# Optimization experiments

Hardware: AMD Instinct MI355X
Metric: run time of the kernel (lower is better)

The kernel has to match this reference:

```python
import jax, jax.numpy as jnp
import numpy as np


def setup_inputs() -> dict:
    key = jax.random.key(0)
    ks = jax.random.split(key, 8)
    n_src, n_dst, n_edges = 100000, 50000, 600000
    d_in, d_out = 128, 128
    n_reuse, n_cache = 5000, 8000
    full_dst_len = n_dst + n_reuse

    feat_src = jax.random.normal(ks[0], (n_src, d_in), jnp.float32)
    src = jax.random.randint(ks[1], (n_edges,), 0, n_src)
    dst = jax.random.randint(ks[2], (n_edges,), 0, n_dst)
    # xavier-ish init for the two bias-free Linear layers (stored as [out, in] like torch)
    W_self = jax.random.normal(ks[3], (d_out, d_in), jnp.float32) / np.sqrt(d_in).astype(np.float32)
    W_neigh = jax.random.normal(ks[4], (d_out, d_in), jnp.float32) / np.sqrt(d_in).astype(np.float32)
    # reuse_indices must be unique positions within [0, full_dst_len)
    reuse_indices = jnp.sort(jax.random.permutation(ks[5], full_dst_len)[:n_reuse])
    reuse_embedding = jax.random.normal(ks[6], (n_reuse, d_out), jnp.float32)
    cache_indices = jax.random.randint(ks[7], (n_cache,), 0, full_dst_len)
    return dict(feat_src=feat_src, W_self=W_self, W_neigh=W_neigh,
                reuse_embedding=reuse_embedding, src=src, dst=dst,
                reuse_indices=reuse_indices, cache_indices=cache_indices,
                n_dst=n_dst)


def reference(feat_src, W_self, W_neigh, reuse_embedding, src, dst,
              reuse_indices, cache_indices, n_dst):
    # --- GraphSAGE 'mean' aggregation on a block graph ---
    feat_dst = feat_src[:n_dst]                         # [n_dst, D_in]
    msgs = feat_src[src]                                # [E, D_in] copy_src gather
    ssum = jax.ops.segment_sum(msgs, dst, num_segments=n_dst)          # [n_dst, D_in]
    deg = jax.ops.segment_sum(jnp.ones_like(msgs[:, 0]), dst, num_segments=n_dst)
    h_neigh = jnp.where(deg[:, None] > 0, ssum / jnp.maximum(deg, 1.0)[:, None], 0.0)
    rst = feat_dst @ W_self.T + h_neigh @ W_neigh.T     # fc_self + fc_neigh

    # --- cache-reuse scatter merge (flag == 0 path) ---
    n_reuse = reuse_indices.shape[0]
    full_dst_len = n_dst + n_reuse
    keep = jnp.ones((full_dst_len,), dtype=bool).at[reuse_indices].set(False)
    unprune_indices = jnp.nonzero(keep, size=n_dst)[0]  # np.delete equivalent
    full = jnp.zeros((full_dst_len, rst.shape[1]), rst.dtype)
    full = full.at[unprune_indices].set(rst).at[reuse_indices].set(reuse_embedding)
    cache_embedding = jax.lax.stop_gradient(full[cache_indices])  # .detach()
    return full, cache_embedding
```

## Files before the change

### kernel.cpp

```cpp
#include <hip/hip_runtime.h>

#define N_SRC   100000
#define N_DST   50000
#define D       128
#define MAXDEG  64

#define RPB     32
#define NB      1563
#define CHUNKS  256
#define TOTAL_BLOCKS 2048
#define COUNT_BLOCKS 256

typedef __attribute__((ext_vector_type(8))) short bf16x8;
typedef __attribute__((ext_vector_type(4))) float f32x4;

__device__ __forceinline__ unsigned short f2bf(float f) {
    unsigned u = __float_as_uint(f);
    u += 0x7FFFu + ((u >> 16) & 1u);
    return (unsigned short)(u >> 16);
}
__device__ __forceinline__ float bf2f(unsigned short u) {
    return __uint_as_float((unsigned)u << 16);
}

__global__ __launch_bounds__(256)
void prep_count_kernel(const int* __restrict__ dst,
                       int* __restrict__ cntmatT,
                       int n_edges, int cb,
                       const int* __restrict__ reuse_idx,
                       int* __restrict__ rowpos, int n_reuse,
                       const float* __restrict__ Wself,
                       const float* __restrict__ Wneigh,
                       unsigned short* __restrict__ wbf,
                       const float* __restrict__ feat,
                       unsigned int* __restrict__ featbf_u32) {
    __shared__ int lc[NB];
    if (blockIdx.x < COUNT_BLOCKS) {
        for (int i = threadIdx.x; i < NB; i += 256) lc[i] = 0;
        __syncthreads();
        int c = blockIdx.x;
        int e0 = c * cb, e1 = min(n_edges, e0 + cb);
        for (int e = e0 + (int)threadIdx.x; e < e1; e += 256)
            atomicAdd(&lc[dst[e] >> 5], 1);
        __syncthreads();
        for (int i = threadIdx.x; i < NB; i += 256)
            cntmatT[i * CHUNKS + c] = lc[i];
    } else {
        int stid = (blockIdx.x - COUNT_BLOCKS) * 256 + threadIdx.x;
        const int sstride = (TOTAL_BLOCKS - COUNT_BLOCKS) * 256;

        if (stid < N_DST) {
            int lo = 0, hi = n_reuse;
            while (lo < hi) {
                int mid = (lo + hi) >> 1;
                if (reuse_idx[mid] - mid > stid) hi = mid; else lo = mid + 1;
            }
            rowpos[stid] = stid + lo;
        }
        if (stid < 128 * 256) {
            int n = stid >> 8;
            int k = stid & 255;
            float v = (k < 128) ? Wself[n * 128 + k] : Wneigh[n * 128 + (k - 128)];
            wbf[stid] = f2bf(v);
        }
        const int n4 = N_SRC * (D / 4);
        for (int i = stid; i < n4; i += sstride) {
            float4 v = *(const float4*)(feat + (size_t)i * 4);
            uint2 o;
            o.x = (unsigned)f2bf(v.x) | ((unsigned)f2bf(v.y) << 16);
            o.y = (unsigned)f2bf(v.z) | ((unsigned)f2bf(v.w) << 16);
            *(uint2*)(featbf_u32 + (size_t)i * 2) = o;
        }
    }
}

__global__ __launch_bounds__(256)
void bucket_scan_kernel(const int* __restrict__ cntmatT,
                        int* __restrict__ offrel,
                        int* __restrict__ bsum) {
    __shared__ int s[CHUNKS];
    int k = blockIdx.x;
    int t = threadIdx.x;
    int x = cntmatT[k * CHUNKS + t];
    s[t] = x;
    __syncthreads();
#pragma unroll
    for (int off = 1; off < CHUNKS; off <<= 1) {
        int v = (t >= off) ? s[t - off] : 0;
        __syncthreads();
        s[t] += v;
        __syncthreads();
    }
    offrel[k * CHUNKS + t] = s[t] - x;
    if (t == CHUNKS - 1) bsum[k] = s[t];
}

__global__ __launch_bounds__(256)
void base_scan_kernel(const int* __restrict__ bsum,
                      int* __restrict__ bucketbase) {
    const int PER = (NB + 255) / 256;
    __shared__ int part[256];
    int t = threadIdx.x;
    int local[PER];
    int run = 0;
#pragma unroll
    for (int i = 0; i < PER; ++i) {
        int idx = t * PER + i;
        int v = (idx < NB) ? bsum[idx] : 0;
        local[i] = run;
        run += v;
    }
    part[t] = run;
    __syncthreads();
#pragma unroll
    for (int off = 1; off < 256; off <<= 1) {
        int v = (t >= off) ? part[t - off] : 0;
        __syncthreads();
        part[t] += v;
        __syncthreads();
    }
    int segbase = part[t] - run;
#pragma unroll
    for (int i = 0; i < PER; ++i) {
        int idx = t * PER + i;
        if (idx < NB) bucketbase[idx] = segbase + local[i];
    }
    if (t == 255) bucketbase[NB] = part[255];
}

__global__ __launch_bounds__(256)
void scatter_kernel(const int* __restrict__ src,
                    const int* __restrict__ dst,
                    const int* __restrict__ offrel,
                    const int* __restrict__ bucketbase,
                    unsigned int* __restrict__ pe,
                    int n_edges, int cb) {
    __shared__ int lc[NB];
    for (int i = threadIdx.x; i < NB; i += 256) lc[i] = 0;
    __syncthreads();
    int c = blockIdx.x;
    int e0 = c * cb, e1 = min(n_edges, e0 + cb);
    for (int e = e0 + (int)threadIdx.x; e < e1; e += 256) {
        int d = dst[e];
        int s = src[e];
        int k = d >> 5;
        int r = atomicAdd(&lc[k], 1);
        int pos = bucketbase[k] + offrel[k * CHUNKS + c] + r;
        pe[pos] = ((unsigned)s << 5) | (unsigned)(d & 31);
    }
}

__global__ __launch_bounds__(256)
void fine_gather_kernel(const unsigned int* __restrict__ pe,
                        const int* __restrict__ bucketbase,
                        const unsigned short* __restrict__ featbf,
                        uint4* __restrict__ hneigh_u4) {
    __shared__ int lell[RPB * MAXDEG];
    __shared__ int rc[RPB];
    int k = blockIdx.x;
    int tid = threadIdx.x;
    if (tid < RPB) rc[tid] = 0;
    __syncthreads();
    int e0 = bucketbase[k], e1 = bucketbase[k + 1];
    for (int e = e0 + tid; e < e1; e += 256) {
        unsigned p = pe[e];
        int rl = (int)(p & 31u);
        int slot = atomicAdd(&rc[rl], 1);
        if (slot < MAXDEG)
            lell[rl * MAXDEG + slot] = (int)(p >> 5);
    }
    __syncthreads();

    union U { uint4 v; unsigned short us[8]; };
#pragma unroll
    for (int pass = 0; pass < 2; ++pass) {
        int rl   = pass * 16 + (tid >> 4);
        int lane = tid & 15;
        int row  = k * RPB + rl;
        if (row < N_DST) {
            int deg = rc[rl];
            int n = min(deg, MAXDEG);
            float inv = 1.0f / fmaxf((float)deg, 1.0f);
            const int* lst = lell + rl * MAXDEG;

            float acc[8];
#pragma unroll
            for (int q = 0; q < 8; ++q) acc[q] = 0.f;

            int j = 0;
            for (; j + 4 <= n; j += 4) {
                int s0 = lst[j + 0];
                int s1 = lst[j + 1];
                int s2 = lst[j + 2];
                int s3 = lst[j + 3];
                U a, b, c, d;
                a.v = *(const uint4*)(featbf + (size_t)s0 * D + lane * 8);
                b.v = *(const uint4*)(featbf + (size_t)s1 * D + lane * 8);
                c.v = *(const uint4*)(featbf + (size_t)s2 * D + lane * 8);
                d.v = *(const uint4*)(featbf + (size_t)s3 * D + lane * 8);
#pragma unroll
                for (int q = 0; q < 8; ++q)
                    acc[q] += (bf2f(a.us[q]) + bf2f(b.us[q])) + (bf2f(c.us[q]) + bf2f(d.us[q]));
            }
            for (; j < n; ++j) {
                int s = lst[j];
                U a;
                a.v = *(const uint4*)(featbf + (size_t)s * D + lane * 8);
#pragma unroll
                for (int q = 0; q < 8; ++q) acc[q] += bf2f(a.us[q]);
            }
            uint4 o;
            o.x = (unsigned)f2bf(acc[0] * inv) | ((unsigned)f2bf(acc[1] * inv) << 16);
            o.y = (unsigned)f2bf(acc[2] * inv) | ((unsigned)f2bf(acc[3] * inv) << 16);
            o.z = (unsigned)f2bf(acc[4] * inv) | ((unsigned)f2bf(acc[5] * inv) << 16);
            o.w = (unsigned)f2bf(acc[6] * inv) | ((unsigned)f2bf(acc[7] * inv) << 16);
            hneigh_u4[(size_t)row * 16 + lane] = o;
        }
    }
}

__global__ __launch_bounds__(256, 2)
void gemm_kernel(const unsigned short* __restrict__ featbf,
                 const unsigned short* __restrict__ hneigh,
                 const unsigned short* __restrict__ wbf,
                 const int* __restrict__ rowpos,
                 float* __restrict__ full) {
    __shared__ unsigned short Wl[128 * 256];

    int tid = threadIdx.x;
    {
        int n = tid >> 1;
        int ckbase = (tid & 1) * 16;
        const uint4* s = (const uint4*)(wbf + n * 256);
        uint4* d = (uint4*)(Wl + n * 256);
#pragma unroll
        for (int i = 0; i < 16; ++i) {
            int ck = ckbase + i;
            d[ck ^ (n & 7)] = s[ck];
        }
    }
    __syncthreads();

    int wv   = tid >> 6;
    int lane = tid & 63;
    int l15  = lane & 15;
    int q    = lane >> 4;
    int rowbase = blockIdx.x * 128 + wv * 32;

    f32x4 acc[2][8];
#pragma unroll
    for (int rt = 0; rt < 2; ++rt)
#pragma unroll
        for (int ct = 0; ct < 8; ++ct) acc[rt][ct] = (f32x4){0.f, 0.f, 0.f, 0.f};

    int r0c = min(rowbase + l15,      N_DST - 1);
    int r1c = min(rowbase + 16 + l15, N_DST - 1);

#pragma unroll
    for (int s = 0; s < 8; ++s) {
        const unsigned short* A = (s < 4) ? featbf : hneigh;
        int k0 = (s & 3) * 32 + q * 8;
        bf16x8 a0 = *(const bf16x8*)(A + (size_t)r0c * D + k0);
        bf16x8 a1 = *(const bf16x8*)(A + (size_t)r1c * D + k0);
#pragma unroll
        for (int ct = 0; ct < 8; ++ct) {
            int n = ct * 16 + l15;
            int ck = s * 4 + q;
            bf16x8 b = *(const bf16x8*)(Wl + n * 256 + ((ck ^ (n & 7)) << 3));
            acc[0][ct] = __builtin_amdgcn_mfma_f32_16x16x32_bf16(a0, b, acc[0][ct], 0, 0, 0);
            acc[1][ct] = __builtin_amdgcn_mfma_f32_16x16x32_bf16(a1, b, acc[1][ct], 0, 0, 0);
        }
    }

#pragma unroll
    for (int rt = 0; rt < 2; ++rt) {
#pragma unroll
        for (int reg = 0; reg < 4; ++reg) {
            int gm = rowbase + rt * 16 + q * 4 + reg;
            if (gm < N_DST) {
                int jj = rowpos[gm];
                float* outr = full + (size_t)jj * D + l15;
#pragma unroll
                for (int ct = 0; ct < 8; ++ct)
                    outr[ct * 16] = acc[rt][ct][reg];
            }
        }
    }
}

__global__ __launch_bounds__(256)
void epilogue_kernel(const float* __restrict__ emb,
                     const int* __restrict__ ridx, int n_reuse,
                     float* __restrict__ full,
                     const int* __restrict__ cidx,
                     float* __restrict__ cache_out, int n_cache) {
    int idx = blockIdx.x * blockDim.x + threadIdx.x;
    int row = idx >> 5;
    int c4 = (idx & 31) * 4;
    if (row < n_reuse) {
        *(float4*)&full[(size_t)ridx[row] * D + c4] =
            *(const float4*)&emb[(size_t)row * D + c4];
    } else if (row < n_reuse + n_cache) {
        int r = row - n_reuse;
        int v = cidx[r];
        int lo = 0, hi = n_reuse;
        while (lo < hi) {
            int mid = (lo + hi) >> 1;
            if (ridx[mid] < v) lo = mid + 1; else hi = mid;
        }
        const float* srcp = (lo < n_reuse && ridx[lo] == v)
            ? emb + (size_t)lo * D
            : full + (size_t)v * D;
        *(float4*)&cache_out[(size_t)r * D + c4] = *(const float4*)&srcp[c4];
    }
}

extern "C" void kernel_launch(void* const* d_in, const int* in_sizes, int n_in,
                              void* d_out, int out_size, void* d_ws, size_t ws_size,
                              hipStream_t stream) {
    const float* feat_src  = (const float*)d_in[0];
    const float* W_self    = (const float*)d_in[1];
    const float* W_neigh   = (const float*)d_in[2];
    const float* reuse_emb = (const float*)d_in[3];
    const int*   src       = (const int*)d_in[4];
    const int*   dst       = (const int*)d_in[5];
    const int*   reuse_idx = (const int*)d_in[6];
    const int*   cache_idx = (const int*)d_in[7];

    int n_edges = in_sizes[4];
    int n_reuse = in_sizes[6];
    int n_cache = in_sizes[7];
    int full_len = N_DST + n_reuse;
    int cb = (n_edges + CHUNKS - 1) / CHUNKS;

    float* full = (float*)d_out;
    float* cache_out = full + (size_t)full_len * D;

    size_t hneigh_b = (size_t)N_DST * D * sizeof(unsigned short);
    size_t featbf_b = (size_t)N_SRC * D * sizeof(unsigned short);

    unsigned short* hneigh = (unsigned short*)d_ws;
    unsigned short* featbf = (unsigned short*)((char*)d_ws + hneigh_b);
    int*   rowpos = (int*)((char*)featbf + featbf_b);
    unsigned short* wbf = (unsigned short*)(rowpos + N_DST);
    int*   cntmatT = (int*)(wbf + 128 * 256);
    int*   offrel  = cntmatT + (size_t)NB * CHUNKS;
    int*   bsum    = offrel + (size_t)NB * CHUNKS;
    int*   bucketbase = bsum + NB;
    unsigned int* pe = (unsigned int*)(bucketbase + NB + 1);

    prep_count_kernel<<<TOTAL_BLOCKS, 256, 0, stream>>>(
        dst, cntmatT, n_edges, cb,
        reuse_idx, rowpos, n_reuse, W_self, W_neigh, wbf,
        feat_src, (unsigned int*)featbf);

    bucket_scan_kernel<<<NB, 256, 0, stream>>>(cntmatT, offrel, bsum);

    base_scan_kernel<<<1, 256, 0, stream>>>(bsum, bucketbase);

    scatter_kernel<<<CHUNKS, 256, 0, stream>>>(
        src, dst, offrel, bucketbase, pe, n_edges, cb);

    fine_gather_kernel<<<NB, 256, 0, stream>>>(
        pe, bucketbase, featbf, (uint4*)hneigh);

    gemm_kernel<<<(N_DST + 127) / 128, 256, 0, stream>>>(
        featbf, hneigh, wbf, rowpos, full);

    epilogue_kernel<<<((n_reuse + n_cache) * 32 + 255) / 256, 256, 0, stream>>>(
        reuse_emb, reuse_idx, n_reuse, full, cache_idx, cache_out, n_cache);
}
```

Measured before the change: 183.6 us.

## Fuse base scan into scatter, move reuse copy into prep, widen gather blocks

Every scatter block now recomputes the bucket-base prefix scan redundantly in shared memory, and block 0 writes it out for later stages. This removes the single-block base_scan launch and its serialization. The reuse-embedding scatter into the full output moves into the prep kernel, so the tail kernel only gathers the cache rows. The fine gather uses 512 threads per block so each thread handles one destination row instead of looping over two passes. The costs are redundant scan work in 256 blocks and more shared memory per scatter block.

```diff
diff --git a/kernel.cpp b/kernel.cpp
--- a/kernel.cpp
+++ b/kernel.cpp
@@ -33,7 +33,9 @@
                        const float* __restrict__ Wneigh,
                        unsigned short* __restrict__ wbf,
                        const float* __restrict__ feat,
-                       unsigned int* __restrict__ featbf_u32) {
+                       unsigned int* __restrict__ featbf_u32,
+                       const float* __restrict__ emb,
+                       float* __restrict__ full) {
     __shared__ int lc[NB];
     if (blockIdx.x < COUNT_BLOCKS) {
         for (int i = threadIdx.x; i < NB; i += 256) lc[i] = 0;
@@ -62,6 +64,12 @@
             int k = stid & 255;
             float v = (k < 128) ? Wself[n * 128 + k] : Wneigh[n * 128 + (k - 128)];
             wbf[stid] = f2bf(v);
+        }
+        for (int i = stid; i < n_reuse * 32; i += sstride) {
+            int r = i >> 5;
+            int c4 = (i & 31) * 4;
+            *(float4*)&full[(size_t)reuse_idx[r] * D + c4] =
+                *(const float4*)&emb[(size_t)r * D + c4];
         }
         const int n4 = N_SRC * (D / 4);
         for (int i = stid; i < n4; i += sstride) {
@@ -96,11 +104,19 @@
 }
 
 __global__ __launch_bounds__(256)
-void base_scan_kernel(const int* __restrict__ bsum,
-                      int* __restrict__ bucketbase) {
+void scatter_kernel(const int* __restrict__ src,
+                    const int* __restrict__ dst,
+                    const int* __restrict__ offrel,
+                    const int* __restrict__ bsum,
+                    int* __restrict__ bucketbase,
+                    unsigned int* __restrict__ pe,
+                    int n_edges, int cb) {
     const int PER = (NB + 255) / 256;
+    __shared__ int bb[NB];
     __shared__ int part[256];
+    __shared__ int lc[NB];
     int t = threadIdx.x;
+
     int local[PER];
     int run = 0;
 #pragma unroll
@@ -123,34 +139,29 @@
 #pragma unroll
     for (int i = 0; i < PER; ++i) {
         int idx = t * PER + i;
-        if (idx < NB) bucketbase[idx] = segbase + local[i];
-    }
-    if (t == 255) bucketbase[NB] = part[255];
-}
-
-__global__ __launch_bounds__(256)
-void scatter_kernel(const int* __restrict__ src,
-                    const int* __restrict__ dst,
-                    const int* __restrict__ offrel,
-                    const int* __restrict__ bucketbase,
-                    unsigned int* __restrict__ pe,
-                    int n_edges, int cb) {
-    __shared__ int lc[NB];
-    for (int i = threadIdx.x; i < NB; i += 256) lc[i] = 0;
-    __syncthreads();
+        if (idx < NB) bb[idx] = segbase + local[i];
+    }
+    for (int i = t; i < NB; i += 256) lc[i] = 0;
+    __syncthreads();
+
+    if (blockIdx.x == 0) {
+        for (int i = t; i < NB; i += 256) bucketbase[i] = bb[i];
+        if (t == 255) bucketbase[NB] = part[255];
+    }
+
     int c = blockIdx.x;
     int e0 = c * cb, e1 = min(n_edges, e0 + cb);
-    for (int e = e0 + (int)threadIdx.x; e < e1; e += 256) {
+    for (int e = e0 + t; e < e1; e += 256) {
         int d = dst[e];
         int s = src[e];
         int k = d >> 5;
         int r = atomicAdd(&lc[k], 1);
-        int pos = bucketbase[k] + offrel[k * CHUNKS + c] + r;
+        int pos = bb[k] + offrel[k * CHUNKS + c] + r;
         pe[pos] = ((unsigned)s << 5) | (unsigned)(d & 31);
     }
 }
 
-__global__ __launch_bounds__(256)
+__global__ __launch_bounds__(512)
 void fine_gather_kernel(const unsigned int* __restrict__ pe,
                         const int* __restrict__ bucketbase,
                         const unsigned short* __restrict__ featbf,
@@ -162,7 +173,7 @@
     if (tid < RPB) rc[tid] = 0;
     __syncthreads();
     int e0 = bucketbase[k], e1 = bucketbase[k + 1];
-    for (int e = e0 + tid; e < e1; e += 256) {
+    for (int e = e0 + tid; e < e1; e += 512) {
         unsigned p = pe[e];
         int rl = (int)(p & 31u);
         int slot = atomicAdd(&rc[rl], 1);
@@ -172,50 +183,47 @@
     __syncthreads();
 
     union U { uint4 v; unsigned short us[8]; };
-#pragma unroll
-    for (int pass = 0; pass < 2; ++pass) {
-        int rl   = pass * 16 + (tid >> 4);
-        int lane = tid & 15;
-        int row  = k * RPB + rl;
-        if (row < N_DST) {
-            int deg = rc[rl];
-            int n = min(deg, MAXDEG);
-            float inv = 1.0f / fmaxf((float)deg, 1.0f);
-            const int* lst = lell + rl * MAXDEG;
-
-            float acc[8];
-#pragma unroll
-            for (int q = 0; q < 8; ++q) acc[q] = 0.f;
-
-            int j = 0;
-            for (; j + 4 <= n; j += 4) {
-                int s0 = lst[j + 0];
-                int s1 = lst[j + 1];
-                int s2 = lst[j + 2];
-                int s3 = lst[j + 3];
-                U a, b, c, d;
-                a.v = *(const uint4*)(featbf + (size_t)s0 * D + lane * 8);
-                b.v = *(const uint4*)(featbf + (size_t)s1 * D + lane * 8);
-                c.v = *(const uint4*)(featbf + (size_t)s2 * D + lane * 8);
-                d.v = *(const uint4*)(featbf + (size_t)s3 * D + lane * 8);
-#pragma unroll
-                for (int q = 0; q < 8; ++q)
-                    acc[q] += (bf2f(a.us[q]) + bf2f(b.us[q])) + (bf2f(c.us[q]) + bf2f(d.us[q]));
-            }
-            for (; j < n; ++j) {
-                int s = lst[j];
-                U a;
-                a.v = *(const uint4*)(featbf + (size_t)s * D + lane * 8);
-#pragma unroll
-                for (int q = 0; q < 8; ++q) acc[q] += bf2f(a.us[q]);
-            }
-            uint4 o;
-            o.x = (unsigned)f2bf(acc[0] * inv) | ((unsigned)f2bf(acc[1] * inv) << 16);
-            o.y = (unsigned)f2bf(acc[2] * inv) | ((unsigned)f2bf(acc[3] * inv) << 16);
-            o.z = (unsigned)f2bf(acc[4] * inv) | ((unsigned)f2bf(acc[5] * inv) << 16);
-            o.w = (unsigned)f2bf(acc[6] * inv) | ((unsigned)f2bf(acc[7] * inv) << 16);
-            hneigh_u4[(size_t)row * 16 + lane] = o;
-        }
+    int rl   = tid >> 4;
+    int lane = tid & 15;
+    int row  = k * RPB + rl;
+    if (row < N_DST) {
+        int deg = rc[rl];
+        int n = min(deg, MAXDEG);
+        float inv = 1.0f / fmaxf((float)deg, 1.0f);
+        const int* lst = lell + rl * MAXDEG;
+
+        float acc[8];
+#pragma unroll
+        for (int q = 0; q < 8; ++q) acc[q] = 0.f;
+
+        int j = 0;
+        for (; j + 4 <= n; j += 4) {
+            int s0 = lst[j + 0];
+            int s1 = lst[j + 1];
+            int s2 = lst[j + 2];
+            int s3 = lst[j + 3];
+            U a, b, c, d;
+            a.v = *(const uint4*)(featbf + (size_t)s0 * D + lane * 8);
+            b.v = *(const uint4*)(featbf + (size_t)s1 * D + lane * 8);
+            c.v = *(const uint4*)(featbf + (size_t)s2 * D + lane * 8);
+            d.v = *(const uint4*)(featbf + (size_t)s3 * D + lane * 8);
+#pragma unroll
+            for (int q = 0; q < 8; ++q)
+                acc[q] += (bf2f(a.us[q]) + bf2f(b.us[q])) + (bf2f(c.us[q]) + bf2f(d.us[q]));
+        }
+        for (; j < n; ++j) {
+            int s = lst[j];
+            U a;
+            a.v = *(const uint4*)(featbf + (size_t)s * D + lane * 8);
+#pragma unroll
+            for (int q = 0; q < 8; ++q) acc[q] += bf2f(a.us[q]);
+        }
+        uint4 o;
+        o.x = (unsigned)f2bf(acc[0] * inv) | ((unsigned)f2bf(acc[1] * inv) << 16);
+        o.y = (unsigned)f2bf(acc[2] * inv) | ((unsigned)f2bf(acc[3] * inv) << 16);
+        o.z = (unsigned)f2bf(acc[4] * inv) | ((unsigned)f2bf(acc[5] * inv) << 16);
+        o.w = (unsigned)f2bf(acc[6] * inv) | ((unsigned)f2bf(acc[7] * inv) << 16);
+        hneigh_u4[(size_t)row * 16 + lane] = o;
     }
 }
 
@@ -289,30 +297,25 @@
 }
 
 __global__ __launch_bounds__(256)
-void epilogue_kernel(const float* __restrict__ emb,
-                     const int* __restrict__ ridx, int n_reuse,
-                     float* __restrict__ full,
-                     const int* __restrict__ cidx,
-                     float* __restrict__ cache_out, int n_cache) {
+void cache_kernel(const float* __restrict__ emb,
+                  const int* __restrict__ ridx, int n_reuse,
+                  const float* __restrict__ full,
+                  const int* __restrict__ cidx,
+                  float* __restrict__ cache_out, int n_cache) {
     int idx = blockIdx.x * blockDim.x + threadIdx.x;
-    int row = idx >> 5;
+    int r = idx >> 5;
+    if (r >= n_cache) return;
     int c4 = (idx & 31) * 4;
-    if (row < n_reuse) {
-        *(float4*)&full[(size_t)ridx[row] * D + c4] =
-            *(const float4*)&emb[(size_t)row * D + c4];
-    } else if (row < n_reuse + n_cache) {
-        int r = row - n_reuse;
-        int v = cidx[r];
-        int lo = 0, hi = n_reuse;
-        while (lo < hi) {
-            int mid = (lo + hi) >> 1;
-            if (ridx[mid] < v) lo = mid + 1; else hi = mid;
-        }
-        const float* srcp = (lo < n_reuse && ridx[lo] == v)
-            ? emb + (size_t)lo * D
-            : full + (size_t)v * D;
-        *(float4*)&cache_out[(size_t)r * D + c4] = *(const float4*)&srcp[c4];
-    }
+    int v = cidx[r];
+    int lo = 0, hi = n_reuse;
+    while (lo < hi) {
+        int mid = (lo + hi) >> 1;
+        if (ridx[mid] < v) lo = mid + 1; else hi = mid;
+    }
+    const float* srcp = (lo < n_reuse && ridx[lo] == v)
+        ? emb + (size_t)lo * D
+        : full + (size_t)v * D;
+    *(float4*)&cache_out[(size_t)r * D + c4] = *(const float4*)&srcp[c4];
 }
 
 extern "C" void kernel_launch(void* const* d_in, const int* in_sizes, int n_in,
@@ -352,21 +355,19 @@
     prep_count_kernel<<<TOTAL_BLOCKS, 256, 0, stream>>>(
         dst, cntmatT, n_edges, cb,
         reuse_idx, rowpos, n_reuse, W_self, W_neigh, wbf,
-        feat_src, (unsigned int*)featbf);
+        feat_src, (unsigned int*)featbf, reuse_emb, full);
 
     bucket_scan_kernel<<<NB, 256, 0, stream>>>(cntmatT, offrel, bsum);
 
-    base_scan_kernel<<<1, 256, 0, stream>>>(bsum, bucketbase);
-
     scatter_kernel<<<CHUNKS, 256, 0, stream>>>(
-        src, dst, offrel, bucketbase, pe, n_edges, cb);
-
-    fine_gather_kernel<<<NB, 256, 0, stream>>>(
+        src, dst, offrel, bsum, bucketbase, pe, n_edges, cb);
+
+    fine_gather_kernel<<<NB, 512, 0, stream>>>(
         pe, bucketbase, featbf, (uint4*)hneigh);
 
     gemm_kernel<<<(N_DST + 127) / 128, 256, 0, stream>>>(
         featbf, hneigh, wbf, rowpos, full);
 
-    epilogue_kernel<<<((n_reuse + n_cache) * 32 + 255) / 256, 256, 0, stream>>>(
+    cache_kernel<<<(n_cache * 32 + 255) / 256, 256, 0, stream>>>(
         reuse_emb, reuse_idx, n_reuse, full, cache_idx, cache_out, n_cache);
 }
```

New measurement: 183.4 us. Within noise of the previous version (-0.1%).
